# Performance work log

Measured on AMD Instinct MI355X. Metric: run time of the kernel, lower is better.

Reference implementation:

```python
import jax, jax.numpy as jnp
import numpy as np
import math

N = 131072          # total points
B = 64              # number of segments (batches)
C = 256             # embedding_dim
H = 8               # num_heads
DH = C // H         # channels per head


def setup_inputs() -> dict:
    key = jax.random.key(0)
    ks = jax.random.split(key, 12)
    q = jax.random.normal(ks[0], (N, C), dtype=jnp.float32)
    k = jax.random.normal(ks[1], (B, C), dtype=jnp.float32)
    v = jax.random.normal(ks[2], (B, C), dtype=jnp.float32)
    batch = jnp.sort(jax.random.randint(ks[3], (N,), 0, B)).astype(jnp.int64)
    s = 1.0 / math.sqrt(C)
    Wq = jax.random.normal(ks[4], (C, C), dtype=jnp.float32) * s
    bq = jnp.zeros((C,), dtype=jnp.float32)
    Wk = jax.random.normal(ks[5], (C, C), dtype=jnp.float32) * s
    bk = jnp.zeros((C,), dtype=jnp.float32)
    Wv = jax.random.normal(ks[6], (C, C), dtype=jnp.float32) * s
    bv = jnp.zeros((C,), dtype=jnp.float32)
    Wo = jax.random.normal(ks[7], (C, C), dtype=jnp.float32) * s
    bo = jnp.zeros((C,), dtype=jnp.float32)
    return {"q": q, "k": k, "v": v, "batch": batch,
            "Wq": Wq, "bq": bq, "Wk": Wk, "bk": bk,
            "Wv": Wv, "bv": bv, "Wo": Wo, "bo": bo}


def reference(q, k, v, batch, Wq, bq, Wk, bk, Wv, bv, Wo, bo):
    batch = batch.astype(jnp.int32)
    # projections (nn.Linear: x @ W.T + b)
    qp = (q @ Wq.T + bq).reshape(N, H, DH)          # [N, H, DH]
    kp = (k @ Wk.T + bk).reshape(B, H, DH)          # [B, H, DH]
    vp = (v @ Wv.T + bv).reshape(B, H, DH)
    # gather per-point k/v by segment id
    kg = kp[batch]                                   # [N, H, DH]
    vg = vp[batch]
    # elementwise attention scores
    attn = qp * kg / math.sqrt(DH)                   # [N, H, DH]
    # ragged per-segment softmax over the point dimension (dim 0 per segment)
    m = jax.ops.segment_max(attn, batch, num_segments=B)   # [B, H, DH]
    e = jnp.exp(attn - m[batch])
    s = jax.ops.segment_sum(e, batch, num_segments=B)      # [B, H, DH]
    a = e / s[batch]                                 # [N, H, DH]
    out = (a * vg).reshape(N, C)                     # weighted values
    return out @ Wo.T + bo
```

## Files before the change

### kernel.cpp

```cpp
#include <hip/hip_runtime.h>
#include <math.h>

#define N_PTS 131072
#define BSEG 64
#define CC 256
#define BM 64
#define NSTEP 8
#define EXP_SHIFT 4.0f

#define INV_SQRT_DH 0.17677669529663687f

typedef short v8s __attribute__((ext_vector_type(8)));
typedef float v4f __attribute__((ext_vector_type(4)));
typedef int   v4i __attribute__((ext_vector_type(4)));

__device__ __forceinline__ float bf2f(unsigned short h) {
    unsigned u = ((unsigned)h) << 16;
    return __builtin_bit_cast(float, u);
}

__device__ __forceinline__ unsigned short f2bf(float f) {
    unsigned u = __builtin_bit_cast(unsigned, f);
    u += 0x7fffu + ((u >> 16) & 1u);
    return (unsigned short)(u >> 16);
}

__device__ __forceinline__ v8s pack8(const float* x) {
    int h2[4];
    #pragma unroll
    for (int i = 0; i < 4; ++i)
        h2[i] = (int)(((unsigned)f2bf(x[2 * i + 1]) << 16) | f2bf(x[2 * i]));
    return __builtin_bit_cast(v8s, make_int4(h2[0], h2[1], h2[2], h2[3]));
}

__device__ __forceinline__ v8s as_v8s(int4 v) { return __builtin_bit_cast(v8s, v); }

__global__ __launch_bounds__(256) void prep_kernel(
    const float* __restrict__ k, const float* __restrict__ v,
    const float* __restrict__ Wk, const float* __restrict__ bk,
    const float* __restrict__ Wv, const float* __restrict__ bv,
    const float* __restrict__ Wq, const float* __restrict__ Wo,
    float* __restrict__ kps, float* __restrict__ vp, float* __restrict__ ssum,
    short* __restrict__ W1q, short* __restrict__ W1o) {
    int bx = blockIdx.x;
    int c = threadIdx.x;
    if (bx < 64) {
        int b = bx;
        const float4* krow  = (const float4*)(k + (size_t)b * CC);
        const float4* vrow  = (const float4*)(v + (size_t)b * CC);
        const float4* wkrow = (const float4*)(Wk + (size_t)c * CC);
        const float4* wvrow = (const float4*)(Wv + (size_t)c * CC);
        float accK = 0.f, accV = 0.f;
        #pragma unroll 8
        for (int i = 0; i < CC / 4; ++i) {
            float4 kk = krow[i], wk = wkrow[i];
            accK += kk.x * wk.x + kk.y * wk.y + kk.z * wk.z + kk.w * wk.w;
            float4 vv = vrow[i], wv = wvrow[i];
            accV += vv.x * wv.x + vv.y * wv.y + vv.z * wv.z + vv.w * wv.w;
        }
        kps[b * CC + c] = (accK + bk[c]) * INV_SQRT_DH;
        vp[b * CC + c] = accV + bv[c];
        ssum[b * CC + c] = 0.f;
    } else {
        int wx = bx - 64;
        const float* W = (wx >= 32) ? Wo : Wq;
        short* W1 = (wx >= 32) ? W1o : W1q;
        int kf = wx & 31;
        const float* src = W + (size_t)c * CC + kf * 8;
        float4 x0 = *(const float4*)(src);
        float4 x1 = *(const float4*)(src + 4);
        float x[8] = {x0.x, x0.y, x0.z, x0.w, x1.x, x1.y, x1.z, x1.w};
        *(v8s*)&W1[((size_t)kf * 256 + c) * 8] = pack8(x);
    }
}

template <int MODE>
__device__ __forceinline__ void gemm_tile(
    char* lds, const int m0,
    const void* __restrict__ Ain, const short* __restrict__ W1,
    const float* __restrict__ bias, void* __restrict__ Outv,
    const int* __restrict__ batch, const float* __restrict__ kps,
    const float* __restrict__ vp, const float* __restrict__ ssum_ro,
    float* __restrict__ ssum) {

    const int tid = threadIdx.x;
    const int lane = tid & 63;
    const int wn = tid >> 6;
    const int kfl = lane >> 4;
    const int rl = lane & 15;
    const int colb = wn * 32;
    const int hsw = ((rl & 7) << 2) | (rl >> 3);

    #pragma unroll
    for (int i = 0; i < 4; ++i) {
        int j = i * 512 + tid;
        int row = j >> 5;
        int ch = j & 31;
        int h = ((row & 7) << 2) | ((row >> 3) & 1);
        int off = row * 512 + ((ch ^ h) << 4);
        if (MODE == 0) {
            const v4f* ap = (const v4f*)((const float*)Ain +
                (size_t)(m0 + row) * CC + ch * 8);
            v4f x0 = __builtin_nontemporal_load(ap);
            v4f x1 = __builtin_nontemporal_load(ap + 1);
            float x[8] = {x0.x, x0.y, x0.z, x0.w, x1.x, x1.y, x1.z, x1.w};
            *(v8s*)(lds + off) = pack8(x);
        } else {
            const v4i* ap = (const v4i*)((const unsigned short*)Ain +
                (size_t)(m0 + row) * CC + ch * 8);
            v4i praw = *ap;
            v8s p = __builtin_bit_cast(v8s, praw);
            int b = batch[m0 + row];
            const float* vpp = vp + (size_t)b * CC + ch * 8;
            const float* ssp = ssum_ro + (size_t)b * CC + ch * 8;
            v4f a0 = *(const v4f*)vpp;
            v4f a1 = *(const v4f*)(vpp + 4);
            v4f s0 = *(const v4f*)ssp;
            v4f s1 = *(const v4f*)(ssp + 4);
            float x[8];
            #pragma unroll
            for (int e = 0; e < 4; ++e) {
                x[e]     = bf2f((unsigned short)p[e]) * __fdividef(a0[e], s0[e]);
                x[4 + e] = bf2f((unsigned short)p[4 + e]) * __fdividef(a1[e], s1[e]);
            }
            *(v8s*)(lds + off) = pack8(x);
        }
    }

    v4f acc[4][2];
    #pragma unroll
    for (int i = 0; i < 4; ++i)
        #pragma unroll
        for (int j = 0; j < 2; ++j) acc[i][j] = (v4f){0.f, 0.f, 0.f, 0.f};

    v8s bcur[2];
    #pragma unroll
    for (int ni = 0; ni < 2; ++ni)
        bcur[ni] = as_v8s(*(const int4*)(W1 +
            ((size_t)kfl * 256 + colb + ni * 16 + rl) * 8));

    __syncthreads();

    #pragma unroll
    for (int s = 0; s < NSTEP; ++s) {
        v8s bnx[2];
        if (s + 1 < NSTEP) {
            #pragma unroll
            for (int ni = 0; ni < 2; ++ni)
                bnx[ni] = as_v8s(*(const int4*)(W1 +
                    ((size_t)((s + 1) * 4 + kfl) * 256 + colb + ni * 16 + rl) * 8));
        }
        #pragma unroll
        for (int mi = 0; mi < 4; ++mi) {
            int abase = (mi * 16 + rl) * 512 + (((s * 4 + kfl) ^ hsw) << 4);
            v8s a = *(const v8s*)(lds + abase);
            #pragma unroll
            for (int ni = 0; ni < 2; ++ni)
                acc[mi][ni] = __builtin_amdgcn_mfma_f32_16x16x32_bf16(
                    a, bcur[ni], acc[mi][ni], 0, 0, 0);
        }
        #pragma unroll
        for (int ni = 0; ni < 2; ++ni) bcur[ni] = bnx[ni];
    }

    __syncthreads();

    const float bb0 = bias[colb + rl];
    const float bb1 = bias[colb + 16 + rl];

    if (MODE == 0) {
        unsigned short* Ou = (unsigned short*)Outv;
        const int bseg = batch[m0];
        const bool fastT = (bseg == batch[m0 + BM - 1]);
        if (!fastT) {
            int curb = -1;
            float r0 = 0.f, r1 = 0.f;
            #pragma unroll
            for (int mi = 0; mi < 4; ++mi)
                #pragma unroll
                for (int r4 = 0; r4 < 4; ++r4) {
                    int row = m0 + mi * 16 + kfl * 4 + r4;
                    int b = batch[row];
                    if (b != curb) {
                        if (curb >= 0) {
                            atomicAdd(&ssum[(size_t)curb * CC + colb + rl], r0);
                            atomicAdd(&ssum[(size_t)curb * CC + colb + 16 + rl], r1);
                            r0 = r1 = 0.f;
                        }
                        curb = b;
                    }
                    float k0 = kps[(size_t)b * CC + colb + rl];
                    float k1 = kps[(size_t)b * CC + colb + 16 + rl];
                    float p0 = __expf((acc[mi][0][r4] + bb0) * k0 - EXP_SHIFT);
                    float p1 = __expf((acc[mi][1][r4] + bb1) * k1 - EXP_SHIFT);
                    Ou[(size_t)row * CC + colb + rl] = f2bf(p0);
                    Ou[(size_t)row * CC + colb + 16 + rl] = f2bf(p1);
                    r0 += p0; r1 += p1;
                }
            atomicAdd(&ssum[(size_t)curb * CC + colb + rl], r0);
            atomicAdd(&ssum[(size_t)curb * CC + colb + 16 + rl], r1);
        } else {
            float k0 = kps[(size_t)bseg * CC + colb + rl];
            float k1 = kps[(size_t)bseg * CC + colb + 16 + rl];
            float cs0 = 0.f, cs1 = 0.f;
            unsigned short* lwu = (unsigned short*)lds + wn * 1024;
            #pragma unroll
            for (int mi = 0; mi < 4; ++mi) {
                #pragma unroll
                for (int r4 = 0; r4 < 4; ++r4) {
                    float p0 = __expf((acc[mi][0][r4] + bb0) * k0 - EXP_SHIFT);
                    float p1 = __expf((acc[mi][1][r4] + bb1) * k1 - EXP_SHIFT);
                    cs0 += p0; cs1 += p1;
                    lwu[(kfl * 4 + r4) * 40 + rl] = f2bf(p0);
                    lwu[(kfl * 4 + r4) * 40 + 16 + rl] = f2bf(p1);
                }
                asm volatile("s_waitcnt lgkmcnt(0)" ::: "memory");
                int row16 = lane >> 2, chunk = lane & 3;
                v4i pv = *(const v4i*)&lwu[row16 * 40 + chunk * 8];
                *(v4i*)&Ou[(size_t)(m0 + mi * 16 + row16) * CC + colb + chunk * 8] = pv;
                asm volatile("s_waitcnt lgkmcnt(0)" ::: "memory");
            }
            cs0 += __shfl_xor(cs0, 16); cs0 += __shfl_xor(cs0, 32);
            cs1 += __shfl_xor(cs1, 16); cs1 += __shfl_xor(cs1, 32);
            if (kfl == 0) {
                atomicAdd(&ssum[(size_t)bseg * CC + colb + rl], cs0);
                atomicAdd(&ssum[(size_t)bseg * CC + colb + 16 + rl], cs1);
            }
        }
    } else {
        float* Of = (float*)Outv;
        float* lwf = (float*)(lds + wn * 2048);
        #pragma unroll
        for (int mi = 0; mi < 4; ++mi)
            #pragma unroll
            for (int c = 0; c < 2; ++c) {
                if ((kfl >> 1) == c) {
                    #pragma unroll
                    for (int r4 = 0; r4 < 4; ++r4) {
                        lwf[((kfl & 1) * 4 + r4) * 36 + rl] = acc[mi][0][r4] + bb0;
                        lwf[((kfl & 1) * 4 + r4) * 36 + 16 + rl] = acc[mi][1][r4] + bb1;
                    }
                }
                asm volatile("s_waitcnt lgkmcnt(0)" ::: "memory");
                int r = lane >> 3, c4 = lane & 7;
                v4f pv = *(const v4f*)&lwf[r * 36 + c4 * 4];
                __builtin_nontemporal_store(pv,
                    (v4f*)&Of[(size_t)(m0 + mi * 16 + c * 8 + r) * CC + colb + c4 * 4]);
                asm volatile("s_waitcnt lgkmcnt(0)" ::: "memory");
            }
    }
}

__global__ __launch_bounds__(512, 4) void gemm_k0(
    const float* __restrict__ q, const short* __restrict__ W1,
    const float* __restrict__ bias, unsigned short* __restrict__ attn,
    const int* __restrict__ batch, const float* __restrict__ kps,
    float* __restrict__ ssum) {
    __shared__ char lds[32768];
    gemm_tile<0>(lds, blockIdx.x * BM, (const void*)q, W1, bias,
                 (void*)attn, batch, kps, nullptr, nullptr, ssum);
}

__global__ __launch_bounds__(512, 4) void gemm_k1(
    const unsigned short* __restrict__ attn, const short* __restrict__ W1,
    const float* __restrict__ bias, float* __restrict__ out,
    const int* __restrict__ batch, const float* __restrict__ vp,
    const float* __restrict__ ssum) {
    __shared__ char lds[32768];
    gemm_tile<1>(lds, blockIdx.x * BM, (const void*)attn, W1, bias,
                 (void*)out, batch, nullptr, vp, ssum, nullptr);
}

extern "C" void kernel_launch(void* const* d_in, const int* in_sizes, int n_in,
                              void* d_out, int out_size, void* d_ws, size_t ws_size,
                              hipStream_t stream) {
    const float* q  = (const float*)d_in[0];
    const float* k  = (const float*)d_in[1];
    const float* v  = (const float*)d_in[2];
    const int* batch = (const int*)d_in[3];
    const float* Wq = (const float*)d_in[4];
    const float* bq = (const float*)d_in[5];
    const float* Wk = (const float*)d_in[6];
    const float* bk = (const float*)d_in[7];
    const float* Wv = (const float*)d_in[8];
    const float* bv = (const float*)d_in[9];
    const float* Wo = (const float*)d_in[10];
    const float* bo = (const float*)d_in[11];
    float* out = (float*)d_out;

    char* wsp = (char*)d_ws;
    unsigned short* attn = (unsigned short*)wsp;
    wsp += (size_t)N_PTS * CC * sizeof(unsigned short);
    float* kps  = (float*)wsp;  wsp += (size_t)BSEG * CC * sizeof(float);
    float* vp   = (float*)wsp;  wsp += (size_t)BSEG * CC * sizeof(float);
    float* ssum = (float*)wsp;  wsp += (size_t)BSEG * CC * sizeof(float);
    short* W1q  = (short*)wsp;  wsp += (size_t)32 * 256 * 8 * sizeof(short);
    short* W1o  = (short*)wsp;  wsp += (size_t)32 * 256 * 8 * sizeof(short);

    prep_kernel<<<128, 256, 0, stream>>>(k, v, Wk, bk, Wv, bv, Wq, Wo,
                                         kps, vp, ssum, W1q, W1o);
    gemm_k0<<<N_PTS / BM, 512, 0, stream>>>(q, W1q, bq, attn, batch, kps, ssum);
    gemm_k1<<<N_PTS / BM, 512, 0, stream>>>(attn, W1o, bo, out, batch, vp, ssum);
}
```

Baseline: 117.8 us.

## Fold per-segment softmax scaling into per-segment Wo copies for uniform tiles

Adds a kernel that builds a bf16 copy of Wo for each segment, scaled by v/sum for that segment, so the output GEMM can skip the per-element scaling of attention values. Tiles whose rows all belong to one segment use the pre-scaled weights and stream their attn rows straight into LDS with global_load_lds. Mixed-segment tiles keep the old path. The cost is an extra launch, 8 MB of extra workspace writes and reads of per-segment weights, and an extra bf16 rounding of the scaled weights.

```diff
diff --git a/kernel.cpp b/kernel.cpp
--- a/kernel.cpp
+++ b/kernel.cpp
@@ -74,6 +74,28 @@
     }
 }
 
+__global__ __launch_bounds__(256) void wo_scale_kernel(
+    const short* __restrict__ W1o, const float* __restrict__ vp,
+    const float* __restrict__ ssum, short* __restrict__ Wos) {
+    int b = blockIdx.x >> 5;
+    int kf = blockIdx.x & 31;
+    int n = threadIdx.x;
+    const float* vpp = vp + (size_t)b * CC + kf * 8;
+    const float* ssp = ssum + (size_t)b * CC + kf * 8;
+    v4f a0 = *(const v4f*)vpp;
+    v4f a1 = *(const v4f*)(vpp + 4);
+    v4f s0 = *(const v4f*)ssp;
+    v4f s1 = *(const v4f*)(ssp + 4);
+    v8s w = *(const v8s*)&W1o[((size_t)kf * 256 + n) * 8];
+    float x[8];
+    #pragma unroll
+    for (int e = 0; e < 4; ++e) {
+        x[e]     = bf2f((unsigned short)w[e]) * __fdividef(a0[e], s0[e]);
+        x[4 + e] = bf2f((unsigned short)w[4 + e]) * __fdividef(a1[e], s1[e]);
+    }
+    *(v8s*)&Wos[(size_t)b * 65536 + ((size_t)kf * 256 + n) * 8] = pack8(x);
+}
+
 template <int MODE>
 __device__ __forceinline__ void gemm_tile(
     char* lds, const int m0,
@@ -91,39 +113,55 @@
     const int colb = wn * 32;
     const int hsw = ((rl & 7) << 2) | (rl >> 3);
 
-    #pragma unroll
-    for (int i = 0; i < 4; ++i) {
-        int j = i * 512 + tid;
-        int row = j >> 5;
-        int ch = j & 31;
-        int h = ((row & 7) << 2) | ((row >> 3) & 1);
-        int off = row * 512 + ((ch ^ h) << 4);
-        if (MODE == 0) {
-            const v4f* ap = (const v4f*)((const float*)Ain +
-                (size_t)(m0 + row) * CC + ch * 8);
-            v4f x0 = __builtin_nontemporal_load(ap);
-            v4f x1 = __builtin_nontemporal_load(ap + 1);
-            float x[8] = {x0.x, x0.y, x0.z, x0.w, x1.x, x1.y, x1.z, x1.w};
-            *(v8s*)(lds + off) = pack8(x);
-        } else {
-            const v4i* ap = (const v4i*)((const unsigned short*)Ain +
-                (size_t)(m0 + row) * CC + ch * 8);
-            v4i praw = *ap;
-            v8s p = __builtin_bit_cast(v8s, praw);
-            int b = batch[m0 + row];
-            const float* vpp = vp + (size_t)b * CC + ch * 8;
-            const float* ssp = ssum_ro + (size_t)b * CC + ch * 8;
-            v4f a0 = *(const v4f*)vpp;
-            v4f a1 = *(const v4f*)(vpp + 4);
-            v4f s0 = *(const v4f*)ssp;
-            v4f s1 = *(const v4f*)(ssp + 4);
-            float x[8];
-            #pragma unroll
-            for (int e = 0; e < 4; ++e) {
-                x[e]     = bf2f((unsigned short)p[e]) * __fdividef(a0[e], s0[e]);
-                x[4 + e] = bf2f((unsigned short)p[4 + e]) * __fdividef(a1[e], s1[e]);
+    if (MODE == 2) {
+        #pragma unroll
+        for (int r = 0; r < 4; ++r) {
+            int row0 = r * 16 + wn * 2;
+            int row = row0 + (lane >> 5);
+            int h = ((row & 7) << 2) | ((row >> 3) & 1);
+            int g16 = (lane & 31) ^ h;
+            const unsigned short* g = (const unsigned short*)Ain +
+                (size_t)(m0 + row) * CC + g16 * 8;
+            __builtin_amdgcn_global_load_lds(
+                (const __attribute__((address_space(1))) void*)g,
+                (__attribute__((address_space(3))) void*)(lds + row0 * 512),
+                16, 0, 0);
+        }
+    } else {
+        #pragma unroll
+        for (int i = 0; i < 4; ++i) {
+            int j = i * 512 + tid;
+            int row = j >> 5;
+            int ch = j & 31;
+            int h = ((row & 7) << 2) | ((row >> 3) & 1);
+            int off = row * 512 + ((ch ^ h) << 4);
+            if (MODE == 0) {
+                const v4f* ap = (const v4f*)((const float*)Ain +
+                    (size_t)(m0 + row) * CC + ch * 8);
+                v4f x0 = __builtin_nontemporal_load(ap);
+                v4f x1 = __builtin_nontemporal_load(ap + 1);
+                float x[8] = {x0.x, x0.y, x0.z, x0.w, x1.x, x1.y, x1.z, x1.w};
+                *(v8s*)(lds + off) = pack8(x);
+            } else {
+                const v4i* ap = (const v4i*)((const unsigned short*)Ain +
+                    (size_t)(m0 + row) * CC + ch * 8);
+                v4i praw = *ap;
+                v8s p = __builtin_bit_cast(v8s, praw);
+                int b = batch[m0 + row];
+                const float* vpp = vp + (size_t)b * CC + ch * 8;
+                const float* ssp = ssum_ro + (size_t)b * CC + ch * 8;
+                v4f a0 = *(const v4f*)vpp;
+                v4f a1 = *(const v4f*)(vpp + 4);
+                v4f s0 = *(const v4f*)ssp;
+                v4f s1 = *(const v4f*)(ssp + 4);
+                float x[8];
+                #pragma unroll
+                for (int e = 0; e < 4; ++e) {
+                    x[e]     = bf2f((unsigned short)p[e]) * __fdividef(a0[e], s0[e]);
+                    x[4 + e] = bf2f((unsigned short)p[4 + e]) * __fdividef(a1[e], s1[e]);
+                }
+                *(v8s*)(lds + off) = pack8(x);
             }
-            *(v8s*)(lds + off) = pack8(x);
         }
     }
 
@@ -262,13 +300,20 @@
 }
 
 __global__ __launch_bounds__(512, 4) void gemm_k1(
-    const unsigned short* __restrict__ attn, const short* __restrict__ W1,
-    const float* __restrict__ bias, float* __restrict__ out,
-    const int* __restrict__ batch, const float* __restrict__ vp,
-    const float* __restrict__ ssum) {
+    const unsigned short* __restrict__ attn, const short* __restrict__ W1o,
+    const short* __restrict__ Wos, const float* __restrict__ bias,
+    float* __restrict__ out, const int* __restrict__ batch,
+    const float* __restrict__ vp, const float* __restrict__ ssum) {
     __shared__ char lds[32768];
-    gemm_tile<1>(lds, blockIdx.x * BM, (const void*)attn, W1, bias,
-                 (void*)out, batch, nullptr, vp, ssum, nullptr);
+    const int m0 = blockIdx.x * BM;
+    const int bseg = batch[m0];
+    if (bseg == batch[m0 + BM - 1]) {
+        gemm_tile<2>(lds, m0, (const void*)attn, Wos + (size_t)bseg * 65536,
+                     bias, (void*)out, batch, nullptr, nullptr, nullptr, nullptr);
+    } else {
+        gemm_tile<1>(lds, m0, (const void*)attn, W1o, bias,
+                     (void*)out, batch, nullptr, vp, ssum, nullptr);
+    }
 }
 
 extern "C" void kernel_launch(void* const* d_in, const int* in_sizes, int n_in,
@@ -296,9 +341,11 @@
     float* ssum = (float*)wsp;  wsp += (size_t)BSEG * CC * sizeof(float);
     short* W1q  = (short*)wsp;  wsp += (size_t)32 * 256 * 8 * sizeof(short);
     short* W1o  = (short*)wsp;  wsp += (size_t)32 * 256 * 8 * sizeof(short);
+    short* Wos  = (short*)wsp;  wsp += (size_t)BSEG * 65536 * sizeof(short);
 
     prep_kernel<<<128, 256, 0, stream>>>(k, v, Wk, bk, Wv, bv, Wq, Wo,
                                          kps, vp, ssum, W1q, W1o);
     gemm_k0<<<N_PTS / BM, 512, 0, stream>>>(q, W1q, bq, attn, batch, kps, ssum);
-    gemm_k1<<<N_PTS / BM, 512, 0, stream>>>(attn, W1o, bo, out, batch, vp, ssum);
-}
+    wo_scale_kernel<<<BSEG * 32, 256, 0, stream>>>(W1o, vp, ssum, Wos);
+    gemm_k1<<<N_PTS / BM, 512, 0, stream>>>(attn, W1o, Wos, bo, out, batch, vp, ssum);
+}
```

Measured after the change: 129.8 us. +10.2%, slower.
